# Kernel optimization log

Hardware: AMD Instinct MI355X
Metric: run time of the kernel (lower is better)

## Reference

```python
import jax, jax.numpy as jnp
import numpy as np

N = 768
SINGLE_DIM = 384
PAIR_DIM = 128
D = 16      # proj_dim per head
H = 12      # n_heads
P = 4       # n_query_points
PV = 8      # n_point_values


def _random_rotations(key, n):
    a = jax.random.normal(key, (n, 3, 3), dtype=jnp.float32)
    q, r = jnp.linalg.qr(a)
    d = jnp.sign(jnp.diagonal(r, axis1=-2, axis2=-1))
    q = q * d[:, None, :]
    det = jnp.linalg.det(q)
    return q * jnp.where(det < 0, -1.0, 1.0)[:, None, None]


def setup_inputs() -> dict:
    key = jax.random.key(0)
    ks = jax.random.split(key, 12)
    s = 0.02
    return {
        "single_rep": jax.random.normal(ks[0], (N, SINGLE_DIM), dtype=jnp.float32),
        "pair_rep": jax.random.normal(ks[1], (N, N, PAIR_DIM), dtype=jnp.float32),
        "rotations": _random_rotations(ks[2], N),
        "translations": jax.random.normal(ks[3], (N, 3), dtype=jnp.float32),
        "Wqkv": s * jax.random.normal(ks[4], (SINGLE_DIM, 3 * H * D), dtype=jnp.float32),
        "Wb": s * jax.random.normal(ks[5], (PAIR_DIM, H), dtype=jnp.float32),
        "Wqk_pts": s * jax.random.normal(ks[6], (SINGLE_DIM, 2 * H * P * 3), dtype=jnp.float32),
        "Wv_pts": s * jax.random.normal(ks[7], (SINGLE_DIM, H * PV * 3), dtype=jnp.float32),
        "gamma": 0.1 * jax.random.normal(ks[8], (H,), dtype=jnp.float32),
        "Wout": s * jax.random.normal(ks[9], (H * (PAIR_DIM + D + PV * 3 + PV), SINGLE_DIM), dtype=jnp.float32),
        "bout": jnp.zeros((SINGLE_DIM,), dtype=jnp.float32),
    }


def _apply_frames(rot, trans, pts):
    # pts: [N, P, H, 3] -> R @ pt + t per residue (dim 0)
    return jnp.einsum('nba,npha->nphb', rot, pts) + trans[:, None, None, :]


def _apply_frames_inv(rot, trans, pts):
    # R^T (pt - t)
    return jnp.einsum('nab,npha->nphb', rot, pts - trans[:, None, None, :])


def reference(single_rep, pair_rep, rotations, translations,
              Wqkv, Wb, Wqk_pts, Wv_pts, gamma, Wout, bout):
    n = single_rep.shape[0]
    sqrt_inv_dim = 1.0 / np.sqrt(D).astype(np.float32)
    w_C = np.sqrt(2.0 / (9.0 * P)).astype(np.float32)
    w_L = np.sqrt(1.0 / 3.0).astype(np.float32)

    qkv = single_rep @ Wqkv                       # [N, 3*H*D]
    q, k, v = jnp.split(qkv, 3, axis=-1)
    q = q.reshape(n, D, H)
    k = k.reshape(n, D, H)
    v = v.reshape(n, D, H)

    b = pair_rep @ Wb                             # [N, N, H]

    qk_pts = single_rep @ Wqk_pts
    q_pts, k_pts = jnp.split(qk_pts, 2, axis=-1)
    q_pts = jnp.moveaxis(q_pts.reshape(n, P, 3, H), -1, -2)   # [N, P, H, 3]
    k_pts = jnp.moveaxis(k_pts.reshape(n, P, 3, H), -1, -2)
    v_pts = jnp.moveaxis((single_rep @ Wv_pts).reshape(n, PV, 3, H), -1, -2)  # [N, PV, H, 3]

    qg = _apply_frames(rotations, translations, q_pts)  # [N, P, H, 3]
    kg = _apply_frames(rotations, translations, k_pts)

    # sum_{p,t} ||qg_i - kg_j||^2 via expansion (avoids [N,N,P,H,3])
    q_sq = jnp.sum(qg * qg, axis=(1, 3))                # [N, H]
    k_sq = jnp.sum(kg * kg, axis=(1, 3))                # [N, H]
    cross = jnp.einsum('ipht,jpht->ijh', qg, kg)        # [N, N, H]
    dist_logits = q_sq[:, None, :] + k_sq[None, :, :] - 2.0 * cross

    dp_logits = sqrt_inv_dim * jnp.einsum('idh,jdh->ijh', q, k) + b
    scale = gamma * (w_C / 2.0)                          # [H]
    a = jax.nn.softmax(w_L * (dp_logits - scale * dist_logits), axis=1)  # [N, N, H]

    out_pair = jnp.einsum('ijh,ijz->izh', a, pair_rep)   # [N, pair_dim, H]
    out_value = jnp.einsum('ijh,jdh->idh', a, v)          # [N, D, H]

    vg = _apply_frames(rotations, translations, v_pts)    # [N, PV, H, 3]
    op = jnp.einsum('ijh,jpht->ipht', a, vg)              # [N, PV, H, 3]
    out_points = _apply_frames_inv(rotations, translations, op)
    out_points_norm = jnp.linalg.norm(out_points, axis=-1)  # [N, PV, H]

    out = jnp.concatenate([
        out_pair.reshape(n, -1),
        out_value.reshape(n, -1),
        out_points.reshape(n, -1),
        out_points_norm.reshape(n, -1),
    ], axis=1)
    return out @ Wout + bout
```

## Files before the change

### kernel.cpp

```cpp
#include <hip/hip_runtime.h>
#include <math.h>

#define NN 768
#define SD 384
#define HH 12

#define W_L 0.57735026918962576f
#define W_C 0.23570226039551584f

typedef __attribute__((ext_vector_type(8))) short short8;
typedef __attribute__((ext_vector_type(4))) short short4_t;
typedef __attribute__((ext_vector_type(4))) float floatx4;
typedef unsigned short ushort_t;
typedef unsigned int uint_t;

__device__ __forceinline__ float wave_max(float v){ for(int o=32;o;o>>=1) v=fmaxf(v,__shfl_xor(v,o)); return v; }
__device__ __forceinline__ float wave_sum(float v){ for(int o=32;o;o>>=1) v+=__shfl_xor(v,o); return v; }

static __device__ __forceinline__ ushort_t f2bf(float f) {
  union { float f; uint_t u; } v; v.f = f;
  uint_t r = (v.u + 0x7FFFu + ((v.u >> 16) & 1u)) >> 16;
  return (ushort_t)r;
}

__global__ __launch_bounds__(256) void k1a_gemm(
    const float* __restrict__ single, const float* __restrict__ Wqkv,
    const float* __restrict__ Wqk, const float* __restrict__ Wvp,
    float* __restrict__ raw)
{
  __shared__ float Al[64][17];
  __shared__ float Bl[16][68];
  const int tid = threadIdx.x;
  const int bm = blockIdx.x / 18, bn = blockIdx.x % 18;
  const int tr = tid >> 4, tc = tid & 15;

  const int bcol = bn*64 + (tid & 15)*4;
  const float* Wsrc; int wstride;
  if (bcol < 576)      { Wsrc = Wqkv + bcol;        wstride = 576; }
  else if (bcol < 864) { Wsrc = Wqk  + (bcol-576);  wstride = 288; }
  else                 { Wsrc = Wvp  + (bcol-864);  wstride = 288; }
  const int brow = tid >> 4;
  const int ar = tid >> 2, ac = (tid & 3)*4;

  float4 acc0 = {0,0,0,0}, acc1 = {0,0,0,0}, acc2 = {0,0,0,0}, acc3 = {0,0,0,0};

  for (int kc = 0; kc < 24; ++kc) {
    __syncthreads();
    *(float4*)&Al[ar][ac] = *(const float4*)(single + (size_t)(bm*64+ar)*SD + kc*16 + ac);
    *(float4*)&Bl[brow][(tid&15)*4] = *(const float4*)(Wsrc + (size_t)(kc*16+brow)*wstride);
    __syncthreads();
    #pragma unroll
    for (int kk = 0; kk < 16; ++kk) {
      float a0 = Al[tr*4+0][kk], a1 = Al[tr*4+1][kk], a2 = Al[tr*4+2][kk], a3 = Al[tr*4+3][kk];
      float4 bv = *(float4*)&Bl[kk][tc*4];
      acc0.x += a0*bv.x; acc0.y += a0*bv.y; acc0.z += a0*bv.z; acc0.w += a0*bv.w;
      acc1.x += a1*bv.x; acc1.y += a1*bv.y; acc1.z += a1*bv.z; acc1.w += a1*bv.w;
      acc2.x += a2*bv.x; acc2.y += a2*bv.y; acc2.z += a2*bv.z; acc2.w += a2*bv.w;
      acc3.x += a3*bv.x; acc3.y += a3*bv.y; acc3.z += a3*bv.z; acc3.w += a3*bv.w;
    }
  }
  float* o = raw + (size_t)(bm*64 + tr*4)*1152 + bn*64 + tc*4;
  *(float4*)(o)            = acc0;
  *(float4*)(o + 1152)     = acc1;
  *(float4*)(o + 2*1152)   = acc2;
  *(float4*)(o + 3*1152)   = acc3;
}

__global__ __launch_bounds__(256) void k1b_pack(
    const float* __restrict__ raw_g, const float* __restrict__ rot,
    const float* __restrict__ trans, const float* __restrict__ gamma,
    float* __restrict__ Qt, ushort_t* __restrict__ Ktb, ushort_t* __restrict__ vvT)
{
  __shared__ float raw[4][1152];
  __shared__ float gbuf[4][16][HH][3];
  const int tid = threadIdx.x;
  const int i0 = blockIdx.x * 4;

  for (int s = tid; s < 4*288; s += 256) {
    int r = s / 288, q = s % 288;
    *(float4*)(&raw[r][q*4]) = *(const float4*)(raw_g + (size_t)(i0+r)*1152 + q*4);
  }
  __syncthreads();

  for (int s = tid; s < 4*576; s += 256) {
    int r = s / 576, cc = s % 576;
    int d = (cc % 192) / HH, h = cc % HH;
    int i = i0 + r;
    float val = raw[r][cc];
    if (cc < 192)       Qt[(size_t)i*384 + h*32 + d] = 0.25f*W_L*val;
    else if (cc < 384)  Ktb[(size_t)i*384 + h*32 + d] = f2bf(val);
    else                vvT[(size_t)(h*40 + d)*768 + i] = f2bf(val);
  }
  for (int s = tid; s < 768; s += 256) {
    int r = s / 192, rem = s % 192;
    int slot = rem / HH, h = rem % HH;
    int i = i0 + r;
    int base;
    if (slot < 4) base = 576 + slot*36;
    else if (slot < 8) base = 720 + (slot-4)*36;
    else base = 864 + (slot-8)*36;
    float x0 = raw[r][base + 0*12 + h];
    float x1 = raw[r][base + 1*12 + h];
    float x2 = raw[r][base + 2*12 + h];
    const float* R = rot + (size_t)i*9;
    const float* T = trans + (size_t)i*3;
    float g0 = R[0]*x0 + R[1]*x1 + R[2]*x2 + T[0];
    float g1 = R[3]*x0 + R[4]*x1 + R[5]*x2 + T[1];
    float g2 = R[6]*x0 + R[7]*x1 + R[8]*x2 + T[2];
    gbuf[r][slot][h][0]=g0; gbuf[r][slot][h][1]=g1; gbuf[r][slot][h][2]=g2;
    if (slot < 4) {
      float sc2 = 2.0f*W_L*(gamma[h]*W_C*0.5f);
      float* q = Qt + (size_t)i*384 + h*32 + 16 + slot*3;
      q[0]=sc2*g0; q[1]=sc2*g1; q[2]=sc2*g2;
    } else if (slot < 8) {
      ushort_t* k = Ktb + (size_t)i*384 + h*32 + 16 + (slot-4)*3;
      k[0]=f2bf(g0); k[1]=f2bf(g1); k[2]=f2bf(g2);
    } else {
      ushort_t* vp = vvT + (size_t)(h*40 + 16 + (slot-8)*3)*768 + i;
      vp[0]=f2bf(g0); vp[768]=f2bf(g1); vp[2*768]=f2bf(g2);
    }
  }
  __syncthreads();
  for (int s = tid; s < 96; s += 256) {
    int r = s / 24, rem = s % 24;
    int h = rem / 2, qk = rem % 2;
    int i = i0 + r;
    float sum = 0;
    int b0 = qk ? 4 : 0;
    for (int p = 0; p < 4; ++p)
      for (int t = 0; t < 3; ++t) { float g = gbuf[r][b0+p][h][t]; sum += g*g; }
    float sc = gamma[h]*W_C*0.5f;
    if (qk == 0) {
      float* q = Qt + (size_t)i*384 + h*32;
      q[28] = -W_L*sc; q[29] = -W_L*sc*sum; q[30] = 0.f; q[31] = 0.f;
    } else {
      ushort_t* k = Ktb + (size_t)i*384 + h*32;
      k[28] = f2bf(sum); k[29] = f2bf(1.f); k[30] = 0; k[31] = 0;
    }
  }
}

__global__ __launch_bounds__(256) void k2a_logits(
    const float* __restrict__ pair, const float* __restrict__ Wb,
    const float* __restrict__ Qt, const ushort_t* __restrict__ Ktb,
    float* __restrict__ L)
{
  __shared__ ushort_t Tj[64*136];
  __shared__ ushort_t WbT[16*136];
  __shared__ float Qrow[384];
  const int tid = threadIdx.x;
  const int i = blockIdx.x / 12;
  const int j0 = (blockIdx.x % 12) * 64;
  const int lane = tid & 63;
  const int w = tid >> 6;
  const int co = lane & 15, gg = lane >> 4;

  for (int s = tid; s < 1536; s += 256) {
    int z = s / 12, h = s % 12;
    WbT[h*136 + z] = f2bf(W_L * Wb[s]);
  }
  for (int s = tid; s < 544; s += 256) WbT[1632 + s] = 0;
  for (int s = tid; s < 384; s += 256) Qrow[s] = Qt[(size_t)i*384 + s];

  const float* src = pair + ((size_t)i*NN + j0)*128;
  #pragma unroll
  for (int k = 0; k < 8; ++k) {
    int f = tid + k*256;
    int row = f >> 5, zq = f & 31;
    float4 v = *(const float4*)(src + (size_t)row*128 + zq*4);
    uint_t u0 = ((uint_t)f2bf(v.y) << 16) | f2bf(v.x);
    uint_t u1 = ((uint_t)f2bf(v.w) << 16) | f2bf(v.z);
    uint_t* d = (uint_t*)&Tj[row*136 + zq*4];
    d[0] = u0; d[1] = u1;
  }
  __syncthreads();

  short8 z8, myQ, wb[4];
  #pragma unroll
  for (int s = 0; s < 8; ++s) z8[s] = 0;
  #pragma unroll
  for (int s = 0; s < 8; ++s)
    myQ[s] = (co < 12) ? (short)f2bf(Qrow[co*32 + gg*8 + s]) : (short)0;
  #pragma unroll
  for (int kt = 0; kt < 4; ++kt)
    wb[kt] = *(const short8*)&WbT[co*136 + kt*32 + gg*8];

  const int jb = w*16;
  floatx4 D; D[0]=0.f; D[1]=0.f; D[2]=0.f; D[3]=0.f;
  #pragma unroll
  for (int kt = 0; kt < 4; ++kt) {
    short8 a = *(const short8*)&Tj[(jb+co)*136 + kt*32 + gg*8];
    D = __builtin_amdgcn_mfma_f32_16x16x32_bf16(a, wb[kt], D, 0, 0, 0);
  }
  const ushort_t* kr = Ktb + (size_t)(j0 + jb + co)*384;
  #pragma unroll
  for (int kt = 0; kt < 12; ++kt) {
    short8 a = *(const short8*)(kr + kt*32 + gg*8);
    short8 b = (co == kt) ? myQ : z8;
    D = __builtin_amdgcn_mfma_f32_16x16x32_bf16(a, b, D, 0, 0, 0);
  }
  if (co < 12) {
    float4 st = {D[0], D[1], D[2], D[3]};
    *(float4*)(L + ((size_t)i*12 + co)*768 + j0 + jb + gg*4) = st;
  }
}

__global__ __launch_bounds__(512) void k3_fused(
    const float* __restrict__ pair, const float* __restrict__ L,
    const ushort_t* __restrict__ vvT, const float* __restrict__ rot,
    const float* __restrict__ trans, float* __restrict__ C2)
{
  __shared__ ushort_t PTb[24*512];
  __shared__ ushort_t Tz[2][2][128*20];
  __shared__ float oacc[480];
  const int tid = threadIdx.x;
  const int i = (NN - 1) - blockIdx.x;
  const int w = tid >> 6, lane = tid & 63;
  const int co = lane & 15, gg = lane >> 4;

  const float* psrc = pair + (size_t)i*NN*128;

  float4 pr0, pr1;
  {
    int f0 = tid,      j0 = f0 >> 5, zq0 = f0 & 31;
    int f1 = tid + 512, j1 = f1 >> 5, zq1 = f1 & 31;
    pr0 = *(const float4*)(psrc + (size_t)j0*128 + zq0*4);
    pr1 = *(const float4*)(psrc + (size_t)j1*128 + zq1*4);
  }

  const float* Lr = L + (size_t)i*12*768;
  #pragma unroll
  for (int m = 0; m < 2; ++m) {
    if (m == 1 && w >= 4) break;
    const int h = (m == 0) ? w : 8 + w;
    const float* row = Lr + (size_t)h*768;
    float mx = -1e30f;
    #pragma unroll
    for (int k = 0; k < 12; ++k) mx = fmaxf(mx, row[lane + 64*k]);
    mx = wave_max(mx);
    float ev[12]; float sm = 0.f;
    #pragma unroll
    for (int k = 0; k < 12; ++k) { ev[k] = __expf(row[lane + 64*k] - mx); sm += ev[k]; }
    sm = wave_sum(sm);
    const float inv = 1.0f / sm;
    #pragma unroll
    for (int k = 0; k < 12; ++k) {
      int jj = lane + 64*k;
      PTb[(jj >> 5)*512 + h*32 + (jj & 31)] = f2bf(ev[k]*inv);
    }
  }
  for (int s = tid; s < 3072; s += 512) {
    int t = s >> 7, rest = s & 127;
    PTb[t*512 + 384 + rest] = 0;
  }

  floatx4 accZ; accZ[0]=0.f; accZ[1]=0.f; accZ[2]=0.f; accZ[3]=0.f;
  floatx4 accV[4];
  #pragma unroll
  for (int u = 0; u < 4; ++u) { accV[u][0]=0.f; accV[u][1]=0.f; accV[u][2]=0.f; accV[u][3]=0.f; }

  const int sw = (w & 3) << 2;
  const int jb = (gg & 1) * 8;
  const ushort_t* vb0 = vvT + (size_t)((w*4+0)*16 + co)*768 + gg*8;
  const ushort_t* vb1 = vvT + (size_t)((w*4+1)*16 + co)*768 + gg*8;
  const ushort_t* vb2 = vvT + (size_t)((w*4+2)*16 + co)*768 + gg*8;
  const ushort_t* vb3 = vvT + (size_t)((w*4+3)*16 + co)*768 + gg*8;

  #pragma unroll 1
  for (int t = 0; t < 24; ++t) {
    const int buf = t & 1;
    {
      int f0 = tid,      j0 = f0 >> 5, zq0 = f0 & 31;
      int f1 = tid + 512, j1 = f1 >> 5, zq1 = f1 & 31;
      const float* p0 = (const float*)&pr0;
      const float* p1 = (const float*)&pr1;
      ushort_t* tz0 = &Tz[buf][j0 >> 4][0];
      ushort_t* tz1 = &Tz[buf][j1 >> 4][0];
      const int jl0 = j0 & 15, jl1 = j1 & 15;
      #pragma unroll
      for (int e = 0; e < 4; ++e) {
        int z0 = zq0*4 + e;
        tz0[z0*20 + (jl0 ^ (((z0 >> 4) & 3) << 2))] = f2bf(p0[e]);
        int z1 = zq1*4 + e;
        tz1[z1*20 + (jl1 ^ (((z1 >> 4) & 3) << 2))] = f2bf(p1[e]);
      }
    }
    if (t < 23) {
      const float* sn = psrc + (size_t)(t+1)*32*128;
      int f0 = tid,      j0 = f0 >> 5, zq0 = f0 & 31;
      int f1 = tid + 512, j1 = f1 >> 5, zq1 = f1 & 31;
      pr0 = *(const float4*)(sn + (size_t)j0*128 + zq0*4);
      pr1 = *(const float4*)(sn + (size_t)j1*128 + zq1*4);
    }
    __syncthreads();

    const short8 aP = *(const short8*)&PTb[t*512 + co*32 + gg*8];
    {
      const ushort_t* tz = &Tz[buf][gg >> 1][0];
      const int zrow = (w*16 + co)*20;
      short4_t lo = *(const short4_t*)&tz[zrow + (jb ^ sw)];
      short4_t hi = *(const short4_t*)&tz[zrow + ((jb + 4) ^ sw)];
      short8 bT;
      #pragma unroll
      for (int e = 0; e < 4; ++e) { bT[e] = lo[e]; bT[e+4] = hi[e]; }
      accZ = __builtin_amdgcn_mfma_f32_16x16x32_bf16(aP, bT, accZ, 0, 0, 0);
    }
    {
      const int toff = t*32;
      short8 bV;
      bV = *(const short8*)(vb0 + toff);
      accV[0] = __builtin_amdgcn_mfma_f32_16x16x32_bf16(aP, bV, accV[0], 0, 0, 0);
      bV = *(const short8*)(vb1 + toff);
      accV[1] = __builtin_amdgcn_mfma_f32_16x16x32_bf16(aP, bV, accV[1], 0, 0, 0);
      if (w*4 + 2 < 30) {
        bV = *(const short8*)(vb2 + toff);
        accV[2] = __builtin_amdgcn_mfma_f32_16x16x32_bf16(aP, bV, accV[2], 0, 0, 0);
        bV = *(const short8*)(vb3 + toff);
        accV[3] = __builtin_amdgcn_mfma_f32_16x16x32_bf16(aP, bV, accV[3], 0, 0, 0);
      }
    }
  }

  float* o = C2 + (size_t)i*2112;
  #pragma unroll
  for (int r = 0; r < 4; ++r) {
    int h = gg*4 + r;
    if (h < 12) o[(w*16 + co)*12 + h] = accZ[r];
  }
  #pragma unroll
  for (int u = 0; u < 4; ++u) {
    int cb = w*4 + u;
    if (cb < 30) {
      int c = cb*16 + co;
      int hc = c / 40;
      #pragma unroll
      for (int r = 0; r < 4; ++r)
        if (gg*4 + r == hc) oacc[c] = accV[u][r];
    }
  }
  __syncthreads();

  if (tid < 96) {
    const int pp = tid / 12, hh = tid % 12;
    const float* R = rot + (size_t)i*9;
    const float* T = trans + (size_t)i*3;
    float x0 = oacc[hh*40+16+pp*3+0] - T[0];
    float x1 = oacc[hh*40+16+pp*3+1] - T[1];
    float x2 = oacc[hh*40+16+pp*3+2] - T[2];
    float y0 = R[0]*x0 + R[3]*x1 + R[6]*x2;
    float y1 = R[1]*x0 + R[4]*x1 + R[7]*x2;
    float y2 = R[2]*x0 + R[5]*x1 + R[8]*x2;
    o[1728 + pp*36 + hh*3 + 0] = y0;
    o[1728 + pp*36 + hh*3 + 1] = y1;
    o[1728 + pp*36 + hh*3 + 2] = y2;
    o[2016 + pp*12 + hh] = sqrtf(y0*y0 + y1*y1 + y2*y2);
  } else if (tid < 288) {
    const int c = tid - 96;
    int d = c / 12, hh = c % 12;
    o[1536 + d*12 + hh] = oacc[hh*40 + d];
  }
}

__global__ __launch_bounds__(256) void k5_out(
    const float* __restrict__ C2, const float* __restrict__ Wout,
    const float* __restrict__ bout, float* __restrict__ out)
{
  __shared__ float Al[32*68];
  __shared__ float Bl[64*36];
  const int tid = threadIdx.x;
  const int bm = blockIdx.x / 12, bn = blockIdx.x % 12;
  const int tr = tid / 16, tc = tid % 16;
  float acc00=0, acc01=0, acc10=0, acc11=0;
  for (int kc = 0; kc < 33; ++kc) {
    __syncthreads();
    for (int s = tid; s < 512; s += 256) {
      int row = s / 16, kq = s % 16;
      *(float4*)(&Al[row*68 + kq*4]) =
        *(const float4*)(C2 + (size_t)(bm*32+row)*2112 + kc*64 + kq*4);
    }
    for (int s = tid; s < 512; s += 256) {
      int kk = s / 8, cq = s % 8;
      *(float4*)(&Bl[kk*36 + cq*4]) =
        *(const float4*)(Wout + (size_t)(kc*64+kk)*384 + bn*32 + cq*4);
    }
    __syncthreads();
    for (int kk = 0; kk < 64; ++kk) {
      float a0 = Al[(tr*2)*68 + kk], a1 = Al[(tr*2+1)*68 + kk];
      float b0 = Bl[kk*36 + tc*2], b1 = Bl[kk*36 + tc*2 + 1];
      acc00 += a0*b0; acc01 += a0*b1;
      acc10 += a1*b0; acc11 += a1*b1;
    }
  }
  int r0 = bm*32 + tr*2, c0 = bn*32 + tc*2;
  out[(size_t)r0*384 + c0]       = acc00 + bout[c0];
  out[(size_t)r0*384 + c0+1]     = acc01 + bout[c0+1];
  out[(size_t)(r0+1)*384 + c0]   = acc10 + bout[c0];
  out[(size_t)(r0+1)*384 + c0+1] = acc11 + bout[c0+1];
}

extern "C" void kernel_launch(void* const* d_in, const int* in_sizes, int n_in,
                              void* d_out, int out_size, void* d_ws, size_t ws_size,
                              hipStream_t stream)
{
  const float* single = (const float*)d_in[0];
  const float* pair   = (const float*)d_in[1];
  const float* rot    = (const float*)d_in[2];
  const float* trans  = (const float*)d_in[3];
  const float* Wqkv   = (const float*)d_in[4];
  const float* Wb     = (const float*)d_in[5];
  const float* Wqk    = (const float*)d_in[6];
  const float* Wvp    = (const float*)d_in[7];
  const float* gamma  = (const float*)d_in[8];
  const float* Wout   = (const float*)d_in[9];
  const float* bout   = (const float*)d_in[10];

  float* ws   = (float*)d_ws;
  float* raw  = ws;
  float* Qt   = raw + (size_t)768*1152;
  float* C2   = Qt  + (size_t)768*384;
  float* L    = C2  + (size_t)768*2112;
  ushort_t* Ktb = (ushort_t*)(L + (size_t)768*12*768);
  ushort_t* vvT = Ktb + (size_t)768*384;
  float* out  = (float*)d_out;

  k1a_gemm<<<dim3(216), dim3(256), 0, stream>>>(single, Wqkv, Wqk, Wvp, raw);
  k1b_pack<<<dim3(192), dim3(256), 0, stream>>>(raw, rot, trans, gamma, Qt, Ktb, vvT);
  k2a_logits<<<dim3(9216), dim3(256), 0, stream>>>(pair, Wb, Qt, Ktb, L);
  k3_fused<<<dim3(768), dim3(512), 0, stream>>>(pair, L, vvT, rot, trans, C2);
  k5_out<<<dim3(288), dim3(256), 0, stream>>>(C2, Wout, bout, out);
}
```

Baseline: 320.0 us.

## Make logits kernel persistent per row with register prefetch; deepen k3 prefetch

```diff
diff --git a/kernel.cpp b/kernel.cpp
--- a/kernel.cpp
+++ b/kernel.cpp
@@ -21,6 +21,9 @@
   union { float f; uint_t u; } v; v.f = f;
   uint_t r = (v.u + 0x7FFFu + ((v.u >> 16) & 1u)) >> 16;
   return (ushort_t)r;
+}
+static __device__ __forceinline__ uint_t pack2bf(float lo, float hi) {
+  return ((uint_t)f2bf(hi) << 16) | (uint_t)f2bf(lo);
 }
 
 __global__ __launch_bounds__(256) void k1a_gemm(
@@ -140,20 +143,20 @@
   }
 }
 
-__global__ __launch_bounds__(256) void k2a_logits(
+__global__ __launch_bounds__(256) void k2p_logits(
     const float* __restrict__ pair, const float* __restrict__ Wb,
     const float* __restrict__ Qt, const ushort_t* __restrict__ Ktb,
     float* __restrict__ L)
 {
-  __shared__ ushort_t Tj[64*136];
+  __shared__ ushort_t Tj[2][64*136];
   __shared__ ushort_t WbT[16*136];
   __shared__ float Qrow[384];
   const int tid = threadIdx.x;
-  const int i = blockIdx.x / 12;
-  const int j0 = (blockIdx.x % 12) * 64;
+  const int i = blockIdx.x;
   const int lane = tid & 63;
   const int w = tid >> 6;
   const int co = lane & 15, gg = lane >> 4;
+  const int srow = tid >> 5, szq = tid & 31;
 
   for (int s = tid; s < 1536; s += 256) {
     int z = s / 12, h = s % 12;
@@ -162,17 +165,12 @@
   for (int s = tid; s < 544; s += 256) WbT[1632 + s] = 0;
   for (int s = tid; s < 384; s += 256) Qrow[s] = Qt[(size_t)i*384 + s];
 
-  const float* src = pair + ((size_t)i*NN + j0)*128;
-  #pragma unroll
-  for (int k = 0; k < 8; ++k) {
-    int f = tid + k*256;
-    int row = f >> 5, zq = f & 31;
-    float4 v = *(const float4*)(src + (size_t)row*128 + zq*4);
-    uint_t u0 = ((uint_t)f2bf(v.y) << 16) | f2bf(v.x);
-    uint_t u1 = ((uint_t)f2bf(v.w) << 16) | f2bf(v.z);
-    uint_t* d = (uint_t*)&Tj[row*136 + zq*4];
-    d[0] = u0; d[1] = u1;
-  }
+  const float* src = pair + (size_t)i*NN*128;
+  float4 pr[8];
+  #pragma unroll
+  for (int k = 0; k < 8; ++k)
+    pr[k] = *(const float4*)(src + (size_t)(srow + k*8)*128 + szq*4);
+
   __syncthreads();
 
   short8 z8, myQ, wb[4];
@@ -186,22 +184,43 @@
     wb[kt] = *(const short8*)&WbT[co*136 + kt*32 + gg*8];
 
   const int jb = w*16;
-  floatx4 D; D[0]=0.f; D[1]=0.f; D[2]=0.f; D[3]=0.f;
-  #pragma unroll
-  for (int kt = 0; kt < 4; ++kt) {
-    short8 a = *(const short8*)&Tj[(jb+co)*136 + kt*32 + gg*8];
-    D = __builtin_amdgcn_mfma_f32_16x16x32_bf16(a, wb[kt], D, 0, 0, 0);
-  }
-  const ushort_t* kr = Ktb + (size_t)(j0 + jb + co)*384;
-  #pragma unroll
-  for (int kt = 0; kt < 12; ++kt) {
-    short8 a = *(const short8*)(kr + kt*32 + gg*8);
-    short8 b = (co == kt) ? myQ : z8;
-    D = __builtin_amdgcn_mfma_f32_16x16x32_bf16(a, b, D, 0, 0, 0);
-  }
-  if (co < 12) {
-    float4 st = {D[0], D[1], D[2], D[3]};
-    *(float4*)(L + ((size_t)i*12 + co)*768 + j0 + jb + gg*4) = st;
+
+  #pragma unroll 1
+  for (int t = 0; t < 12; ++t) {
+    const int buf = t & 1;
+    #pragma unroll
+    for (int k = 0; k < 8; ++k) {
+      uint2 uu;
+      uu.x = pack2bf(pr[k].x, pr[k].y);
+      uu.y = pack2bf(pr[k].z, pr[k].w);
+      *(uint2*)&Tj[buf][(srow + k*8)*136 + szq*4] = uu;
+    }
+    if (t < 11) {
+      const float* sn = src + (size_t)(t+1)*64*128;
+      #pragma unroll
+      for (int k = 0; k < 8; ++k)
+        pr[k] = *(const float4*)(sn + (size_t)(srow + k*8)*128 + szq*4);
+    }
+    __syncthreads();
+
+    floatx4 D; D[0]=0.f; D[1]=0.f; D[2]=0.f; D[3]=0.f;
+    #pragma unroll
+    for (int kt = 0; kt < 4; ++kt) {
+      short8 a = *(const short8*)&Tj[buf][(jb+co)*136 + kt*32 + gg*8];
+      D = __builtin_amdgcn_mfma_f32_16x16x32_bf16(a, wb[kt], D, 0, 0, 0);
+    }
+    const ushort_t* kr = Ktb + (size_t)(t*64 + jb + co)*384;
+    #pragma unroll
+    for (int kt = 0; kt < 12; ++kt) {
+      short8 a = *(const short8*)(kr + kt*32 + gg*8);
+      short8 b = (co == kt) ? myQ : z8;
+      D = __builtin_amdgcn_mfma_f32_16x16x32_bf16(a, b, D, 0, 0, 0);
+    }
+    if (co < 12) {
+      float4 st = {D[0], D[1], D[2], D[3]};
+      *(float4*)(L + ((size_t)i*12 + co)*768 + t*64 + jb + gg*4) = st;
+    }
+    __syncthreads();
   }
 }
 
@@ -219,14 +238,14 @@
   const int co = lane & 15, gg = lane >> 4;
 
   const float* psrc = pair + (size_t)i*NN*128;
-
-  float4 pr0, pr1;
-  {
-    int f0 = tid,      j0 = f0 >> 5, zq0 = f0 & 31;
-    int f1 = tid + 512, j1 = f1 >> 5, zq1 = f1 & 31;
-    pr0 = *(const float4*)(psrc + (size_t)j0*128 + zq0*4);
-    pr1 = *(const float4*)(psrc + (size_t)j1*128 + zq1*4);
-  }
+  const int f0 = tid,       pj0 = f0 >> 5, pz0 = f0 & 31;
+  const int f1 = tid + 512, pj1 = f1 >> 5, pz1 = f1 & 31;
+
+  float4 pa0, pa1, pb0, pb1;
+  pa0 = *(const float4*)(psrc + (size_t)pj0*128 + pz0*4);
+  pa1 = *(const float4*)(psrc + (size_t)pj1*128 + pz1*4);
+  pb0 = *(const float4*)(psrc + (size_t)(32 + pj0)*128 + pz0*4);
+  pb1 = *(const float4*)(psrc + (size_t)(32 + pj1)*128 + pz1*4);
 
   const float* Lr = L + (size_t)i*12*768;
   #pragma unroll
@@ -266,31 +285,26 @@
   const ushort_t* vb2 = vvT + (size_t)((w*4+2)*16 + co)*768 + gg*8;
   const ushort_t* vb3 = vvT + (size_t)((w*4+3)*16 + co)*768 + gg*8;
 
-  #pragma unroll 1
-  for (int t = 0; t < 24; ++t) {
+  auto ITER = [&](int t, float4& r0, float4& r1) {
     const int buf = t & 1;
     {
-      int f0 = tid,      j0 = f0 >> 5, zq0 = f0 & 31;
-      int f1 = tid + 512, j1 = f1 >> 5, zq1 = f1 & 31;
-      const float* p0 = (const float*)&pr0;
-      const float* p1 = (const float*)&pr1;
-      ushort_t* tz0 = &Tz[buf][j0 >> 4][0];
-      ushort_t* tz1 = &Tz[buf][j1 >> 4][0];
-      const int jl0 = j0 & 15, jl1 = j1 & 15;
+      const float* p0 = (const float*)&r0;
+      const float* p1 = (const float*)&r1;
+      ushort_t* tz0 = &Tz[buf][pj0 >> 4][0];
+      ushort_t* tz1 = &Tz[buf][pj1 >> 4][0];
+      const int jl0 = pj0 & 15, jl1 = pj1 & 15;
       #pragma unroll
       for (int e = 0; e < 4; ++e) {
-        int z0 = zq0*4 + e;
+        int z0 = pz0*4 + e;
         tz0[z0*20 + (jl0 ^ (((z0 >> 4) & 3) << 2))] = f2bf(p0[e]);
-        int z1 = zq1*4 + e;
+        int z1 = pz1*4 + e;
         tz1[z1*20 + (jl1 ^ (((z1 >> 4) & 3) << 2))] = f2bf(p1[e]);
       }
     }
-    if (t < 23) {
-      const float* sn = psrc + (size_t)(t+1)*32*128;
-      int f0 = tid,      j0 = f0 >> 5, zq0 = f0 & 31;
-      int f1 = tid + 512, j1 = f1 >> 5, zq1 = f1 & 31;
-      pr0 = *(const float4*)(sn + (size_t)j0*128 + zq0*4);
-      pr1 = *(const float4*)(sn + (size_t)j1*128 + zq1*4);
+    if (t < 22) {
+      const float* sn = psrc + (size_t)(t+2)*32*128;
+      r0 = *(const float4*)(sn + (size_t)pj0*128 + pz0*4);
+      r1 = *(const float4*)(sn + (size_t)pj1*128 + pz1*4);
     }
     __syncthreads();
 
@@ -319,6 +333,13 @@
         accV[3] = __builtin_amdgcn_mfma_f32_16x16x32_bf16(aP, bV, accV[3], 0, 0, 0);
       }
     }
+    __syncthreads();
+  };
+
+  #pragma unroll 1
+  for (int tt = 0; tt < 24; tt += 2) {
+    ITER(tt,     pa0, pa1);
+    ITER(tt + 1, pb0, pb1);
   }
 
   float* o = C2 + (size_t)i*2112;
@@ -425,7 +446,7 @@
 
   k1a_gemm<<<dim3(216), dim3(256), 0, stream>>>(single, Wqkv, Wqk, Wvp, raw);
   k1b_pack<<<dim3(192), dim3(256), 0, stream>>>(raw, rot, trans, gamma, Qt, Ktb, vvT);
-  k2a_logits<<<dim3(9216), dim3(256), 0, stream>>>(pair, Wb, Qt, Ktb, L);
+  k2p_logits<<<dim3(768), dim3(256), 0, stream>>>(pair, Wb, Qt, Ktb, L);
   k3_fused<<<dim3(768), dim3(512), 0, stream>>>(pair, L, vvT, rot, trans, C2);
   k5_out<<<dim3(288), dim3(256), 0, stream>>>(C2, Wout, bout, out);
 }
```

After: 338.2 us. +5.7%, slower.

## Emit transposed bf16 pair tile from logits kernel and consume it in attention kernel

Applied to the files above, without the earlier changes.

```diff
diff --git a/kernel.cpp b/kernel.cpp
--- a/kernel.cpp
+++ b/kernel.cpp
@@ -9,7 +9,6 @@
 #define W_C 0.23570226039551584f
 
 typedef __attribute__((ext_vector_type(8))) short short8;
-typedef __attribute__((ext_vector_type(4))) short short4_t;
 typedef __attribute__((ext_vector_type(4))) float floatx4;
 typedef unsigned short ushort_t;
 typedef unsigned int uint_t;
@@ -21,6 +20,9 @@
   union { float f; uint_t u; } v; v.f = f;
   uint_t r = (v.u + 0x7FFFu + ((v.u >> 16) & 1u)) >> 16;
   return (ushort_t)r;
+}
+static __device__ __forceinline__ uint_t pack2bf(float lo, float hi) {
+  return ((uint_t)f2bf(hi) << 16) | (uint_t)f2bf(lo);
 }
 
 __global__ __launch_bounds__(256) void k1a_gemm(
@@ -140,10 +142,10 @@
   }
 }
 
-__global__ __launch_bounds__(256) void k2a_logits(
+__global__ __launch_bounds__(256) void k2t_logits(
     const float* __restrict__ pair, const float* __restrict__ Wb,
     const float* __restrict__ Qt, const ushort_t* __restrict__ Ktb,
-    float* __restrict__ L)
+    float* __restrict__ L, ushort_t* __restrict__ Tzg)
 {
   __shared__ ushort_t Tj[64*136];
   __shared__ ushort_t WbT[16*136];
@@ -163,15 +165,20 @@
   for (int s = tid; s < 384; s += 256) Qrow[s] = Qt[(size_t)i*384 + s];
 
   const float* src = pair + ((size_t)i*NN + j0)*128;
+  float4 pv[8];
   #pragma unroll
   for (int k = 0; k < 8; ++k) {
     int f = tid + k*256;
     int row = f >> 5, zq = f & 31;
-    float4 v = *(const float4*)(src + (size_t)row*128 + zq*4);
-    uint_t u0 = ((uint_t)f2bf(v.y) << 16) | f2bf(v.x);
-    uint_t u1 = ((uint_t)f2bf(v.w) << 16) | f2bf(v.z);
+    pv[k] = *(const float4*)(src + (size_t)row*128 + zq*4);
+  }
+  #pragma unroll
+  for (int k = 0; k < 8; ++k) {
+    int f = tid + k*256;
+    int row = f >> 5, zq = f & 31;
     uint_t* d = (uint_t*)&Tj[row*136 + zq*4];
-    d[0] = u0; d[1] = u1;
+    d[0] = pack2bf(pv[k].x, pv[k].y);
+    d[1] = pack2bf(pv[k].z, pv[k].w);
   }
   __syncthreads();
 
@@ -203,30 +210,34 @@
     float4 st = {D[0], D[1], D[2], D[3]};
     *(float4*)(L + ((size_t)i*12 + co)*768 + j0 + jb + gg*4) = st;
   }
-}
-
-__global__ __launch_bounds__(512) void k3_fused(
-    const float* __restrict__ pair, const float* __restrict__ L,
+
+  const int z = tid & 127, jg = tid >> 7;
+  uint_t ow[16];
+  #pragma unroll
+  for (int m = 0; m < 16; ++m) {
+    ushort_t a = Tj[(jg*32 + 2*m)*136 + z];
+    ushort_t b = Tj[(jg*32 + 2*m + 1)*136 + z];
+    ow[m] = ((uint_t)b << 16) | (uint_t)a;
+  }
+  ushort_t* dst = Tzg + ((size_t)i*128 + z)*768 + j0 + jg*32;
+  #pragma unroll
+  for (int q = 0; q < 4; ++q) {
+    uint4 u4 = {ow[q*4+0], ow[q*4+1], ow[q*4+2], ow[q*4+3]};
+    *(uint4*)(dst + q*8) = u4;
+  }
+}
+
+__global__ __launch_bounds__(512) void k3g(
+    const float* __restrict__ L, const ushort_t* __restrict__ Tzg,
     const ushort_t* __restrict__ vvT, const float* __restrict__ rot,
     const float* __restrict__ trans, float* __restrict__ C2)
 {
   __shared__ ushort_t PTb[24*512];
-  __shared__ ushort_t Tz[2][2][128*20];
   __shared__ float oacc[480];
   const int tid = threadIdx.x;
   const int i = (NN - 1) - blockIdx.x;
   const int w = tid >> 6, lane = tid & 63;
   const int co = lane & 15, gg = lane >> 4;
-
-  const float* psrc = pair + (size_t)i*NN*128;
-
-  float4 pr0, pr1;
-  {
-    int f0 = tid,      j0 = f0 >> 5, zq0 = f0 & 31;
-    int f1 = tid + 512, j1 = f1 >> 5, zq1 = f1 & 31;
-    pr0 = *(const float4*)(psrc + (size_t)j0*128 + zq0*4);
-    pr1 = *(const float4*)(psrc + (size_t)j1*128 + zq1*4);
-  }
 
   const float* Lr = L + (size_t)i*12*768;
   #pragma unroll
@@ -253,71 +264,46 @@
     int t = s >> 7, rest = s & 127;
     PTb[t*512 + 384 + rest] = 0;
   }
+  __syncthreads();
 
   floatx4 accZ; accZ[0]=0.f; accZ[1]=0.f; accZ[2]=0.f; accZ[3]=0.f;
   floatx4 accV[4];
   #pragma unroll
   for (int u = 0; u < 4; ++u) { accV[u][0]=0.f; accV[u][1]=0.f; accV[u][2]=0.f; accV[u][3]=0.f; }
 
-  const int sw = (w & 3) << 2;
-  const int jb = (gg & 1) * 8;
+  const bool full = (w*4 + 2 < 30);
+  const ushort_t* tz  = Tzg + ((size_t)i*128 + w*16 + co)*768 + gg*8;
   const ushort_t* vb0 = vvT + (size_t)((w*4+0)*16 + co)*768 + gg*8;
   const ushort_t* vb1 = vvT + (size_t)((w*4+1)*16 + co)*768 + gg*8;
   const ushort_t* vb2 = vvT + (size_t)((w*4+2)*16 + co)*768 + gg*8;
   const ushort_t* vb3 = vvT + (size_t)((w*4+3)*16 + co)*768 + gg*8;
 
+  short8 nT  = *(const short8*)(tz);
+  short8 nV0 = *(const short8*)(vb0);
+  short8 nV1 = *(const short8*)(vb1);
+  short8 nV2 = nT, nV3 = nT;
+  if (full) { nV2 = *(const short8*)(vb2); nV3 = *(const short8*)(vb3); }
+
   #pragma unroll 1
   for (int t = 0; t < 24; ++t) {
-    const int buf = t & 1;
-    {
-      int f0 = tid,      j0 = f0 >> 5, zq0 = f0 & 31;
-      int f1 = tid + 512, j1 = f1 >> 5, zq1 = f1 & 31;
-      const float* p0 = (const float*)&pr0;
-      const float* p1 = (const float*)&pr1;
-      ushort_t* tz0 = &Tz[buf][j0 >> 4][0];
-      ushort_t* tz1 = &Tz[buf][j1 >> 4][0];
-      const int jl0 = j0 & 15, jl1 = j1 & 15;
-      #pragma unroll
-      for (int e = 0; e < 4; ++e) {
-        int z0 = zq0*4 + e;
-        tz0[z0*20 + (jl0 ^ (((z0 >> 4) & 3) << 2))] = f2bf(p0[e]);
-        int z1 = zq1*4 + e;
-        tz1[z1*20 + (jl1 ^ (((z1 >> 4) & 3) << 2))] = f2bf(p1[e]);
+    short8 cT = nT, cV0 = nV0, cV1 = nV1, cV2 = nV2, cV3 = nV3;
+    if (t < 23) {
+      const int toff = (t+1)*32;
+      nT  = *(const short8*)(tz  + toff);
+      nV0 = *(const short8*)(vb0 + toff);
+      nV1 = *(const short8*)(vb1 + toff);
+      if (full) {
+        nV2 = *(const short8*)(vb2 + toff);
+        nV3 = *(const short8*)(vb3 + toff);
       }
     }
-    if (t < 23) {
-      const float* sn = psrc + (size_t)(t+1)*32*128;
-      int f0 = tid,      j0 = f0 >> 5, zq0 = f0 & 31;
-      int f1 = tid + 512, j1 = f1 >> 5, zq1 = f1 & 31;
-      pr0 = *(const float4*)(sn + (size_t)j0*128 + zq0*4);
-      pr1 = *(const float4*)(sn + (size_t)j1*128 + zq1*4);
-    }
-    __syncthreads();
-
     const short8 aP = *(const short8*)&PTb[t*512 + co*32 + gg*8];
-    {
-      const ushort_t* tz = &Tz[buf][gg >> 1][0];
-      const int zrow = (w*16 + co)*20;
-      short4_t lo = *(const short4_t*)&tz[zrow + (jb ^ sw)];
-      short4_t hi = *(const short4_t*)&tz[zrow + ((jb + 4) ^ sw)];
-      short8 bT;
-      #pragma unroll
-      for (int e = 0; e < 4; ++e) { bT[e] = lo[e]; bT[e+4] = hi[e]; }
-      accZ = __builtin_amdgcn_mfma_f32_16x16x32_bf16(aP, bT, accZ, 0, 0, 0);
-    }
-    {
-      const int toff = t*32;
-      short8 bV;
-      bV = *(const short8*)(vb0 + toff);
-      accV[0] = __builtin_amdgcn_mfma_f32_16x16x32_bf16(aP, bV, accV[0], 0, 0, 0);
-      bV = *(const short8*)(vb1 + toff);
-      accV[1] = __builtin_amdgcn_mfma_f32_16x16x32_bf16(aP, bV, accV[1], 0, 0, 0);
-      if (w*4 + 2 < 30) {
-        bV = *(const short8*)(vb2 + toff);
-        accV[2] = __builtin_amdgcn_mfma_f32_16x16x32_bf16(aP, bV, accV[2], 0, 0, 0);
-        bV = *(const short8*)(vb3 + toff);
-        accV[3] = __builtin_amdgcn_mfma_f32_16x16x32_bf16(aP, bV, accV[3], 0, 0, 0);
-      }
+    accZ    = __builtin_amdgcn_mfma_f32_16x16x32_bf16(aP, cT,  accZ,    0, 0, 0);
+    accV[0] = __builtin_amdgcn_mfma_f32_16x16x32_bf16(aP, cV0, accV[0], 0, 0, 0);
+    accV[1] = __builtin_amdgcn_mfma_f32_16x16x32_bf16(aP, cV1, accV[1], 0, 0, 0);
+    if (full) {
+      accV[2] = __builtin_amdgcn_mfma_f32_16x16x32_bf16(aP, cV2, accV[2], 0, 0, 0);
+      accV[3] = __builtin_amdgcn_mfma_f32_16x16x32_bf16(aP, cV3, accV[3], 0, 0, 0);
     }
   }
 
@@ -421,11 +407,12 @@
   float* L    = C2  + (size_t)768*2112;
   ushort_t* Ktb = (ushort_t*)(L + (size_t)768*12*768);
   ushort_t* vvT = Ktb + (size_t)768*384;
+  ushort_t* Tzg = vvT + (size_t)480*768;
   float* out  = (float*)d_out;
 
   k1a_gemm<<<dim3(216), dim3(256), 0, stream>>>(single, Wqkv, Wqk, Wvp, raw);
   k1b_pack<<<dim3(192), dim3(256), 0, stream>>>(raw, rot, trans, gamma, Qt, Ktb, vvT);
-  k2a_logits<<<dim3(9216), dim3(256), 0, stream>>>(pair, Wb, Qt, Ktb, L);
-  k3_fused<<<dim3(768), dim3(512), 0, stream>>>(pair, L, vvT, rot, trans, C2);
+  k2t_logits<<<dim3(9216), dim3(256), 0, stream>>>(pair, Wb, Qt, Ktb, L, Tzg);
+  k3g<<<dim3(768), dim3(512), 0, stream>>>(L, Tzg, vvT, rot, trans, C2);
   k5_out<<<dim3(288), dim3(256), 0, stream>>>(C2, Wout, bout, out);
 }
```

Result: slower. 373.5 us (+16.7%).
